# Kernel tuning notes

Hardware: AMD Instinct MI355X
Metric: run time of the kernel (lower is better)

The kernel has to match this reference:

```python
import jax, jax.numpy as jnp
import numpy as np

N_NODES = 100000
N_EDGES = 3200000
D_FEAT = 128
HIDDEN = 128
BN_EPS = 1e-3  # Keras BatchNormalization default epsilon


def setup_inputs() -> dict:
    key = jax.random.key(0)
    k = jax.random.split(key, 8)
    H = jax.random.normal(k[0], (N_NODES, D_FEAT), dtype=jnp.float32)
    edge_src = jax.random.randint(k[1], (N_EDGES,), 0, N_NODES, dtype=jnp.int32)
    edge_dst = jax.random.randint(k[2], (N_EDGES,), 0, N_NODES, dtype=jnp.int32)
    edge_w = jax.random.uniform(k[3], (N_EDGES,), dtype=jnp.float32)
    # BatchNorm (inference-mode) parameters
    gamma = jnp.ones((D_FEAT,), dtype=jnp.float32)
    beta = jnp.zeros((D_FEAT,), dtype=jnp.float32)
    moving_mean = 0.1 * jax.random.normal(k[4], (D_FEAT,), dtype=jnp.float32)
    moving_var = jnp.abs(1.0 + 0.1 * jax.random.normal(k[5], (D_FEAT,), dtype=jnp.float32))
    # Dense layer params
    W = jax.random.normal(k[6], (D_FEAT, HIDDEN), dtype=jnp.float32) / np.sqrt(D_FEAT)
    b = jnp.zeros((HIDDEN,), dtype=jnp.float32)
    return {
        "H": H, "edge_src": edge_src, "edge_dst": edge_dst, "edge_w": edge_w,
        "gamma": gamma, "beta": beta, "moving_mean": moving_mean,
        "moving_var": moving_var, "W": W, "b": b, "num_nodes": N_NODES,
    }


def reference(H, edge_src, edge_dst, edge_w, gamma, beta, moving_mean, moving_var, W, b, num_nodes):
    # Sparse adjacency SpMM: h[dst] += w * H[src]
    msgs = H[edge_src] * edge_w[:, None]                      # [E, d]
    h = jax.ops.segment_sum(msgs, edge_dst, num_segments=num_nodes)  # [N, d]
    # BatchNorm (inference) -> Dropout (identity at inference) -> Dense + exact GELU
    h = (h - moving_mean) * jax.lax.rsqrt(moving_var + BN_EPS) * gamma + beta
    out = jax.nn.gelu(h @ W + b, approximate=False)           # [N, hidden]
    return out
```

## Files before the change

### kernel.cpp

```cpp
#include <hip/hip_runtime.h>
#include <math.h>


#define DF 128
#define SCAN_ELEMS 1024
#define BKSH 6
#define BKNODES (1 << BKSH)
#define NB 128
#define CAP 4096

typedef short short8 __attribute__((ext_vector_type(8)));
typedef float f32x4 __attribute__((ext_vector_type(4)));

__device__ __forceinline__ unsigned short f32_to_bf16_rne(float f) {
  unsigned u = __float_as_uint(f);
  return (unsigned short)((u + 0x7FFFu + ((u >> 16) & 1u)) >> 16);
}

__global__ __launch_bounds__(256) void scatter_kernel(
    const float* __restrict__ H, const int* __restrict__ esrc,
    const int* __restrict__ edst, const float* __restrict__ ew,
    float* __restrict__ h, int E) {
  int tid = blockIdx.x * blockDim.x + threadIdx.x;
  int e = tid >> 5;
  int lane = tid & 31;
  if (e >= E) return;
  int s = esrc[e];
  int d = edst[e];
  float w = ew[e];
  const float4* Hs = reinterpret_cast<const float4*>(H + (size_t)s * DF);
  float4 v = Hs[lane];
  float* hd = h + (size_t)d * DF + lane * 4;
  atomicAdd(hd + 0, v.x * w);
  atomicAdd(hd + 1, v.y * w);
  atomicAdd(hd + 2, v.z * w);
  atomicAdd(hd + 3, v.w * w);
}

__global__ __launch_bounds__(256) void convert_bf16_kernel(
    const float4* __restrict__ H4, ushort4* __restrict__ Hb, int n4) {
  int i = blockIdx.x * blockDim.x + threadIdx.x;
  if (i >= n4) return;
  float4 v = H4[i];
  ushort4 o;
  o.x = f32_to_bf16_rne(v.x);
  o.y = f32_to_bf16_rne(v.y);
  o.z = f32_to_bf16_rne(v.z);
  o.w = f32_to_bf16_rne(v.w);
  Hb[i] = o;
}

__global__ __launch_bounds__(256) void prep_w2frag_kernel(
    const float* __restrict__ W, const float* __restrict__ gamma,
    const float* __restrict__ var, unsigned short* __restrict__ W2frag) {
  int idx = blockIdx.x * blockDim.x + threadIdx.x;
  int i = idx & 7;
  int l = (idx >> 3) & 63;
  int kt = (idx >> 9) & 3;
  int ct = idx >> 11;
  int k = kt * 32 + (l >> 4) * 8 + i;
  int c = ct * 16 + (l & 15);
  float s = gamma[k] * rsqrtf(var[k] + 1e-3f);
  W2frag[idx] = f32_to_bf16_rne(s * W[(size_t)k * DF + c]);
}

__global__ __launch_bounds__(128) void prep_bias2_kernel(
    const float* __restrict__ W, const float* __restrict__ gamma,
    const float* __restrict__ beta, const float* __restrict__ mean,
    const float* __restrict__ var, const float* __restrict__ b,
    float* __restrict__ bias2) {
  int c = threadIdx.x;
  float acc = b[c];
  for (int k = 0; k < DF; ++k) {
    float s = gamma[k] * rsqrtf(var[k] + 1e-3f);
    float t = beta[k] - mean[k] * s;
    acc += t * W[(size_t)k * DF + c];
  }
  bias2[c] = acc;
}

__global__ __launch_bounds__(512) void hist_blk_kernel(
    const int* __restrict__ edst, int* __restrict__ bcnt,
    int E, int nbk, int chunk) {
  extern __shared__ int hcnt[];
  int b = blockIdx.x;
  int t = threadIdx.x;
  for (int i = t; i < nbk; i += 512) hcnt[i] = 0;
  __syncthreads();
  int e0 = b * chunk;
  int e1 = min(E, e0 + chunk);
  for (int e = e0 + t; e < e1; e += 512)
    atomicAdd(&hcnt[edst[e] >> BKSH], 1);
  __syncthreads();
  for (int k = t; k < nbk; k += 512)
    bcnt[(size_t)k * NB + b] = hcnt[k];
}

__global__ __launch_bounds__(256) void scan1_kernel(
    const int* __restrict__ cnt, int* __restrict__ pre,
    int* __restrict__ bsum, int N) {
  __shared__ int s[256];
  int t = threadIdx.x;
  int base = blockIdx.x * SCAN_ELEMS + t * 4;
  int v0 = (base + 0 < N) ? cnt[base + 0] : 0;
  int v1 = (base + 1 < N) ? cnt[base + 1] : 0;
  int v2 = (base + 2 < N) ? cnt[base + 2] : 0;
  int v3 = (base + 3 < N) ? cnt[base + 3] : 0;
  int tsum = v0 + v1 + v2 + v3;
  s[t] = tsum;
  __syncthreads();
  for (int off = 1; off < 256; off <<= 1) {
    int tmp = (t >= off) ? s[t - off] : 0;
    __syncthreads();
    s[t] += tmp;
    __syncthreads();
  }
  int run = s[t] - tsum;
  if (base + 0 < N) pre[base + 0] = run;
  run += v0;
  if (base + 1 < N) pre[base + 1] = run;
  run += v1;
  if (base + 2 < N) pre[base + 2] = run;
  run += v2;
  if (base + 3 < N) pre[base + 3] = run;
  if (t == 255) bsum[blockIdx.x] = s[255];
}

__global__ __launch_bounds__(256) void scan2_kernel(int* __restrict__ bsum, int nb) {
  __shared__ int s[256];
  int t = threadIdx.x;
  int v = (t < nb) ? bsum[t] : 0;
  s[t] = v;
  __syncthreads();
  for (int off = 1; off < 256; off <<= 1) {
    int tmp = (t >= off) ? s[t - off] : 0;
    __syncthreads();
    s[t] += tmp;
    __syncthreads();
  }
  if (t < nb) bsum[t] = s[t] - v;
  if (t == 255) bsum[nb] = s[255];
}

__global__ __launch_bounds__(256) void scan3_kernel(
    int* __restrict__ gbase, const int* __restrict__ bsum, int NBKG, int nb) {
  int i = blockIdx.x * blockDim.x + threadIdx.x;
  if (i < NBKG) gbase[i] += bsum[i >> 10];
  if (i == 0) gbase[NBKG] = bsum[nb];
}

__global__ __launch_bounds__(512) void scatter_blk_kernel(
    const int* __restrict__ esrc, const int* __restrict__ edst,
    const float* __restrict__ ew, const int* __restrict__ gbase,
    uint2* __restrict__ payload, int E, int nbk, int chunk) {
  extern __shared__ int cur[];
  int b = blockIdx.x;
  int t = threadIdx.x;
  for (int k = t; k < nbk; k += 512) cur[k] = gbase[(size_t)k * NB + b];
  __syncthreads();
  int e0 = b * chunk;
  int e1 = min(E, e0 + chunk);
  for (int e = e0 + t; e < e1; e += 512) {
    int d = edst[e];
    int k = d >> BKSH;
    int pos = atomicAdd(&cur[k], 1);
    uint2 v;
    v.x = (unsigned)esrc[e] | ((unsigned)(d & (BKNODES - 1)) << 17);
    v.y = __float_as_uint(ew[e]);
    payload[pos] = v;
  }
}

__global__ __launch_bounds__(256) void reorder2_kernel(
    const uint2* __restrict__ payload, const int* __restrict__ gbase,
    uint2* __restrict__ csr, int* __restrict__ rowptr,
    int N, int nbk, int E) {
  __shared__ uint2 stage[CAP];
  __shared__ int cnt[BKNODES];
  __shared__ int s64[BKNODES];
  __shared__ int cur[BKNODES];
  int bk = blockIdx.x;
  int t = threadIdx.x;
  int base = gbase[(size_t)bk * NB];
  int end  = gbase[(size_t)(bk + 1) * NB];
  int len = end - base;
  bool fit = (len <= CAP);

  if (t < BKNODES) cnt[t] = 0;
  __syncthreads();
  if (fit) {
    for (int j = t; j < len; j += 256) {
      uint2 m = payload[base + j];
      stage[j] = m;
      atomicAdd(&cnt[m.x >> 17], 1);
    }
  } else {
    for (int j = t; j < len; j += 256)
      atomicAdd(&cnt[payload[base + j].x >> 17], 1);
  }
  __syncthreads();
  if (t < BKNODES) s64[t] = cnt[t];
  __syncthreads();
  for (int off = 1; off < BKNODES; off <<= 1) {
    int tmp = 0;
    if (t < BKNODES && t >= off) tmp = s64[t - off];
    __syncthreads();
    if (t < BKNODES) s64[t] += tmp;
    __syncthreads();
  }
  if (t < BKNODES) {
    int ex = s64[t] - cnt[t];
    cur[t] = ex;
    int node = (bk << BKSH) + t;
    if (node < N) rowptr[node] = base + ex;
  }
  if (bk == nbk - 1 && t == 0) rowptr[N] = E;
  __syncthreads();
  if (fit) {
    for (int j = t; j < len; j += 256) {
      uint2 m = stage[j];
      int dl = (int)(m.x >> 17);
      int pos = atomicAdd(&cur[dl], 1);
      uint2 o;
      o.x = m.x & 0x1FFFFu;
      o.y = m.y;
      csr[(size_t)base + pos] = o;
    }
  } else {
    for (int j = t; j < len; j += 256) {
      uint2 m = payload[base + j];
      int dl = (int)(m.x >> 17);
      int pos = atomicAdd(&cur[dl], 1);
      uint2 o;
      o.x = m.x & 0x1FFFFu;
      o.y = m.y;
      csr[(size_t)base + pos] = o;
    }
  }
}

__global__ __launch_bounds__(256) void pull_csr_b_kernel(
    const unsigned* __restrict__ Hb, const int* __restrict__ rowptr,
    const uint2* __restrict__ csr_sw, unsigned* __restrict__ hb_out, int N) {
  int wave = threadIdx.x >> 6;
  int lane = threadIdx.x & 63;
  int node = blockIdx.x * 4 + wave;
  if (node >= N) return;

  int rs = rowptr[node];
  int re = rowptr[node + 1];
  float ax = 0.0f, ay = 0.0f;

  int j = rs;
  for (; j + 8 <= re; j += 8) {
    uint2 m[8];
#pragma unroll
    for (int k = 0; k < 8; ++k) m[k] = csr_sw[j + k];
    float lo[8], hi[8];
#pragma unroll
    for (int k = 0; k < 8; ++k) {
      unsigned p = Hb[(size_t)m[k].x * 64 + lane];
      lo[k] = __uint_as_float(p << 16);
      hi[k] = __uint_as_float(p & 0xFFFF0000u);
    }
#pragma unroll
    for (int k = 0; k < 8; ++k) {
      float w = __uint_as_float(m[k].y);
      ax = fmaf(lo[k], w, ax);
      ay = fmaf(hi[k], w, ay);
    }
  }
  for (; j < re; ++j) {
    uint2 m = csr_sw[j];
    float w = __uint_as_float(m.y);
    unsigned p = Hb[(size_t)m.x * 64 + lane];
    ax = fmaf(__uint_as_float(p << 16), w, ax);
    ay = fmaf(__uint_as_float(p & 0xFFFF0000u), w, ay);
  }

  unsigned pack = (unsigned)f32_to_bf16_rne(ax) |
                  ((unsigned)f32_to_bf16_rne(ay) << 16);
  hb_out[(size_t)node * 64 + lane] = pack;
}

__global__ __launch_bounds__(256) void pull_csr_f32_kernel(
    const float2* __restrict__ H2, const int* __restrict__ rowptr,
    const uint2* __restrict__ csr_sw, float* __restrict__ h, int N) {
  int wave = threadIdx.x >> 6;
  int lane = threadIdx.x & 63;
  int node = blockIdx.x * 4 + wave;
  if (node >= N) return;
  int rs = rowptr[node];
  int re = rowptr[node + 1];
  float ax = 0.0f, ay = 0.0f;
  for (int j = rs; j < re; ++j) {
    uint2 m = csr_sw[j];
    float w = __uint_as_float(m.y);
    float2 u = H2[(size_t)m.x * 64 + lane];
    ax = fmaf(u.x, w, ax);
    ay = fmaf(u.y, w, ay);
  }
  float2 r;
  r.x = ax;
  r.y = ay;
  reinterpret_cast<float2*>(h)[(size_t)node * 64 + lane] = r;
}

__global__ __launch_bounds__(256) void mfma_gemm_gelu_kernel(
    const unsigned short* __restrict__ hb,
    const unsigned short* __restrict__ W2frag,
    const float* __restrict__ bias2,
    float* __restrict__ out, int N) {
  __shared__ unsigned short sW[8 * 4 * 64 * 8];

  int t = threadIdx.x;
  {
    const uint4* src = (const uint4*)W2frag;
    uint4* dst = (uint4*)sW;
    for (int i = t; i < 2048; i += 256) dst[i] = src[i];
  }
  __syncthreads();

  int wid = t >> 6;
  int l = t & 63;
  int row0 = blockIdx.x * 64 + wid * 16;

  int arow = row0 + (l & 15);
  if (arow >= N) arow = N - 1;
  const short8* hrow = (const short8*)(hb + (size_t)arow * DF);
  int asub = l >> 4;
  short8 a[4];
#pragma unroll
  for (int kt = 0; kt < 4; ++kt) a[kt] = hrow[kt * 4 + asub];

  const short8* wf = (const short8*)sW;
  int orow = (l >> 4) * 4;
  int ocol = l & 15;

#pragma unroll
  for (int ct = 0; ct < 8; ++ct) {
    f32x4 acc = {0.0f, 0.0f, 0.0f, 0.0f};
#pragma unroll
    for (int kt = 0; kt < 4; ++kt) {
      short8 bfr = wf[(ct * 4 + kt) * 64 + l];
      acc = __builtin_amdgcn_mfma_f32_16x16x32_bf16(a[kt], bfr, acc, 0, 0, 0);
    }
    int col = ct * 16 + ocol;
    float bb = bias2[col];
#pragma unroll
    for (int r = 0; r < 4; ++r) {
      int row = row0 + orow + r;
      if (row < N) {
        float x = acc[r] + bb;
        float g = 0.5f * x * (1.0f + erff(x * 0.70710678118654752440f));
        out[(size_t)row * DF + col] = g;
      }
    }
  }
}

__global__ __launch_bounds__(256) void fused_bn_gemm_gelu(
    float* __restrict__ hout, const float* __restrict__ gamma,
    const float* __restrict__ beta, const float* __restrict__ mean,
    const float* __restrict__ var, const float* __restrict__ W,
    const float* __restrict__ b, int N) {
  __shared__ float s_s[DF];
  __shared__ float s_t[DF];
  __shared__ float s_hb[16][DF];
  __shared__ float s_W[32][DF];

  int t = threadIdx.x;
  if (t < DF) {
    float sv = gamma[t] * rsqrtf(var[t] + 1e-3f);
    s_s[t] = sv;
    s_t[t] = beta[t] - mean[t] * sv;
  }
  __syncthreads();

  int n0 = blockIdx.x * 16;
  for (int i = t; i < 16 * DF; i += 256) {
    int r = i >> 7;
    int c = i & (DF - 1);
    int node = n0 + r;
    float hv = (node < N) ? hout[(size_t)node * DF + c] : 0.0f;
    s_hb[r][c] = hv * s_s[c] + s_t[c];
  }

  float acc[8];
#pragma unroll
  for (int i = 0; i < 8; i++) acc[i] = 0.0f;

  int col = t & (DF - 1);
  int half = t >> 7;

  for (int kc = 0; kc < DF; kc += 32) {
    __syncthreads();
    for (int i = t; i < 32 * DF; i += 256) {
      int r = i >> 7;
      int c = i & (DF - 1);
      s_W[r][c] = W[(size_t)(kc + r) * DF + c];
    }
    __syncthreads();
#pragma unroll
    for (int kk = 0; kk < 32; kk++) {
      float wv = s_W[kk][col];
#pragma unroll
      for (int i = 0; i < 8; i++) {
        acc[i] += s_hb[half + i * 2][kc + kk] * wv;
      }
    }
  }

  float bb = b[col];
#pragma unroll
  for (int i = 0; i < 8; i++) {
    int node = n0 + half + i * 2;
    if (node < N) {
      float x = acc[i] + bb;
      float g = 0.5f * x * (1.0f + erff(x * 0.70710678118654752440f));
      hout[(size_t)node * DF + col] = g;
    }
  }
}

extern "C" void kernel_launch(void* const* d_in, const int* in_sizes, int n_in,
                              void* d_out, int out_size, void* d_ws, size_t ws_size,
                              hipStream_t stream) {
  const float* H     = (const float*)d_in[0];
  const int*   esrc  = (const int*)d_in[1];
  const int*   edst  = (const int*)d_in[2];
  const float* ew    = (const float*)d_in[3];
  const float* gamma = (const float*)d_in[4];
  const float* beta  = (const float*)d_in[5];
  const float* mean  = (const float*)d_in[6];
  const float* var   = (const float*)d_in[7];
  const float* W     = (const float*)d_in[8];
  const float* b     = (const float*)d_in[9];

  int N = in_sizes[0] / DF;
  int E = in_sizes[1];
  float* h = (float*)d_out;

  int nbk = (N + BKNODES - 1) / BKNODES;
  int NBKG = nbk * NB;
  int nbA = (NBKG + SCAN_ELEMS - 1) / SCAN_ELEMS;
  int chunk = (E + NB - 1) / NB;

  size_t off = 0;
  auto alloc = [&](size_t bytes) {
    size_t o = off;
    off += (bytes + 255) & ~(size_t)255;
    return o;
  };
  size_t o_bcnt   = alloc((size_t)NBKG * 4);
  size_t o_gbase  = alloc((size_t)(NBKG + 1) * 4);
  size_t o_bsum   = alloc((size_t)(nbA + 1) * 4);
  size_t o_rowptr = alloc((size_t)(N + 1) * 4);
  size_t o_w2     = alloc((size_t)16384 * 2);
  size_t o_bias2  = alloc((size_t)DF * 4);
  size_t o_pl     = alloc((size_t)E * 8);
  size_t o_csr    = alloc((size_t)E * 8);
  size_t need_bin = off;
  size_t o_hb     = alloc((size_t)N * DF * 2);
  size_t need_bf16 = off;

  char* ws = (char*)d_ws;

  if (ws_size >= need_bin) {
    int* bcnt    = (int*)(ws + o_bcnt);
    int* gbase   = (int*)(ws + o_gbase);
    int* bsum    = (int*)(ws + o_bsum);
    int* rowptr  = (int*)(ws + o_rowptr);
    unsigned short* W2frag = (unsigned short*)(ws + o_w2);
    float* bias2 = (float*)(ws + o_bias2);
    uint2* payload = (uint2*)(ws + o_pl);
    uint2* csr     = (uint2*)(ws + o_csr);
    bool tierA = (ws_size >= need_bf16 && (size_t)N * DF * 2 <= (size_t)E * 8);

    size_t lds_bytes = (size_t)nbk * 4;

    if (tierA) {
      ushort4* Hb = (ushort4*)(ws + o_hb);
      int n4 = N * DF / 4;
      convert_bf16_kernel<<<(n4 + 255) / 256, 256, 0, stream>>>(
          (const float4*)H, Hb, n4);
      prep_w2frag_kernel<<<64, 256, 0, stream>>>(W, gamma, var, W2frag);
      prep_bias2_kernel<<<1, 128, 0, stream>>>(W, gamma, beta, mean, var, b,
                                               bias2);
      hist_blk_kernel<<<NB, 512, lds_bytes, stream>>>(edst, bcnt, E, nbk, chunk);
      scan1_kernel<<<nbA, 256, 0, stream>>>(bcnt, gbase, bsum, NBKG);
      scan2_kernel<<<1, 256, 0, stream>>>(bsum, nbA);
      scan3_kernel<<<(NBKG + 256) / 256, 256, 0, stream>>>(gbase, bsum, NBKG, nbA);
      scatter_blk_kernel<<<NB, 512, lds_bytes, stream>>>(esrc, edst, ew, gbase,
                                                         payload, E, nbk, chunk);
      reorder2_kernel<<<nbk, 256, 0, stream>>>(payload, gbase, csr, rowptr,
                                               N, nbk, E);
      unsigned* hb_out = (unsigned*)(ws + o_pl);
      pull_csr_b_kernel<<<(N + 3) / 4, 256, 0, stream>>>(
          (const unsigned*)Hb, rowptr, csr, hb_out, N);
      mfma_gemm_gelu_kernel<<<(N + 63) / 64, 256, 0, stream>>>(
          (const unsigned short*)hb_out, W2frag, bias2, (float*)d_out, N);
    } else {
      hist_blk_kernel<<<NB, 512, lds_bytes, stream>>>(edst, bcnt, E, nbk, chunk);
      scan1_kernel<<<nbA, 256, 0, stream>>>(bcnt, gbase, bsum, NBKG);
      scan2_kernel<<<1, 256, 0, stream>>>(bsum, nbA);
      scan3_kernel<<<(NBKG + 256) / 256, 256, 0, stream>>>(gbase, bsum, NBKG, nbA);
      scatter_blk_kernel<<<NB, 512, lds_bytes, stream>>>(esrc, edst, ew, gbase,
                                                         payload, E, nbk, chunk);
      reorder2_kernel<<<nbk, 256, 0, stream>>>(payload, gbase, csr, rowptr,
                                               N, nbk, E);
      pull_csr_f32_kernel<<<(N + 3) / 4, 256, 0, stream>>>(
          (const float2*)H, rowptr, csr, h, N);
      fused_bn_gemm_gelu<<<(N + 15) / 16, 256, 0, stream>>>(h, gamma, beta,
                                                            mean, var, W, b, N);
    }
  } else {
    hipMemsetAsync(d_out, 0, (size_t)out_size * sizeof(float), stream);
    long long threads = (long long)E * 32;
    long long grid = (threads + 255) / 256;
    scatter_kernel<<<(int)grid, 256, 0, stream>>>(H, esrc, edst, ew, h, E);
    fused_bn_gemm_gelu<<<(N + 15) / 16, 256, 0, stream>>>(h, gamma, beta,
                                                          mean, var, W, b, N);
  }
}
```

Measured before the change: 258.1 us.

## Fuse bucket reorder with CSR pull and merge prep/scan kernels

Replaces the separate reorder-to-CSR and pull kernels with one kernel that counting-sorts each 64-node bucket in shared memory and immediately gathers bf16 features for those nodes, avoiding the global CSR/rowptr write and reread. Also merges the three prep kernels into one launch and scan2/scan3 into one kernel that recomputes the block-sum scan per block. Trades global traffic and launches for large 1024-thread blocks with 48KB LDS, which may reduce occupancy; oversized buckets fall back to a slow linear scan path.

```diff
diff --git a/kernel.cpp b/kernel.cpp
--- a/kernel.cpp
+++ b/kernel.cpp
@@ -8,6 +8,7 @@
 #define BKNODES (1 << BKSH)
 #define NB 128
 #define CAP 4096
+#define CAP2 3072
 
 typedef short short8 __attribute__((ext_vector_type(8)));
 typedef float f32x4 __attribute__((ext_vector_type(4)));
@@ -37,63 +38,58 @@
   atomicAdd(hd + 3, v.w * w);
 }
 
-__global__ __launch_bounds__(256) void convert_bf16_kernel(
-    const float4* __restrict__ H4, ushort4* __restrict__ Hb, int n4) {
-  int i = blockIdx.x * blockDim.x + threadIdx.x;
-  if (i >= n4) return;
-  float4 v = H4[i];
-  ushort4 o;
-  o.x = f32_to_bf16_rne(v.x);
-  o.y = f32_to_bf16_rne(v.y);
-  o.z = f32_to_bf16_rne(v.z);
-  o.w = f32_to_bf16_rne(v.w);
-  Hb[i] = o;
-}
-
-__global__ __launch_bounds__(256) void prep_w2frag_kernel(
-    const float* __restrict__ W, const float* __restrict__ gamma,
-    const float* __restrict__ var, unsigned short* __restrict__ W2frag) {
-  int idx = blockIdx.x * blockDim.x + threadIdx.x;
-  int i = idx & 7;
-  int l = (idx >> 3) & 63;
-  int kt = (idx >> 9) & 3;
-  int ct = idx >> 11;
-  int k = kt * 32 + (l >> 4) * 8 + i;
-  int c = ct * 16 + (l & 15);
-  float s = gamma[k] * rsqrtf(var[k] + 1e-3f);
-  W2frag[idx] = f32_to_bf16_rne(s * W[(size_t)k * DF + c]);
-}
-
-__global__ __launch_bounds__(128) void prep_bias2_kernel(
+__global__ __launch_bounds__(256) void prep_all_kernel(
+    const float4* __restrict__ H4, ushort4* __restrict__ Hb, int n4,
     const float* __restrict__ W, const float* __restrict__ gamma,
     const float* __restrict__ beta, const float* __restrict__ mean,
     const float* __restrict__ var, const float* __restrict__ b,
-    float* __restrict__ bias2) {
-  int c = threadIdx.x;
-  float acc = b[c];
-  for (int k = 0; k < DF; ++k) {
+    unsigned short* __restrict__ W2frag, float* __restrict__ bias2) {
+  int idx = blockIdx.x * blockDim.x + threadIdx.x;
+  if (idx < n4) {
+    float4 v = H4[idx];
+    ushort4 o;
+    o.x = f32_to_bf16_rne(v.x);
+    o.y = f32_to_bf16_rne(v.y);
+    o.z = f32_to_bf16_rne(v.z);
+    o.w = f32_to_bf16_rne(v.w);
+    Hb[idx] = o;
+  }
+  if (idx < 16384) {
+    int i = idx & 7;
+    int l = (idx >> 3) & 63;
+    int kt = (idx >> 9) & 3;
+    int ct = idx >> 11;
+    int k = kt * 32 + (l >> 4) * 8 + i;
+    int c = ct * 16 + (l & 15);
     float s = gamma[k] * rsqrtf(var[k] + 1e-3f);
-    float t = beta[k] - mean[k] * s;
-    acc += t * W[(size_t)k * DF + c];
-  }
-  bias2[c] = acc;
+    W2frag[idx] = f32_to_bf16_rne(s * W[(size_t)k * DF + c]);
+  } else if (idx < 16384 + DF) {
+    int c = idx - 16384;
+    float acc = b[c];
+    for (int k = 0; k < DF; ++k) {
+      float s = gamma[k] * rsqrtf(var[k] + 1e-3f);
+      float t = beta[k] - mean[k] * s;
+      acc += t * W[(size_t)k * DF + c];
+    }
+    bias2[c] = acc;
+  }
 }
 
 __global__ __launch_bounds__(512) void hist_blk_kernel(
     const int* __restrict__ edst, int* __restrict__ bcnt,
     int E, int nbk, int chunk) {
   extern __shared__ int hcnt[];
-  int b = blockIdx.x;
+  int bblk = blockIdx.x;
   int t = threadIdx.x;
   for (int i = t; i < nbk; i += 512) hcnt[i] = 0;
   __syncthreads();
-  int e0 = b * chunk;
+  int e0 = bblk * chunk;
   int e1 = min(E, e0 + chunk);
   for (int e = e0 + t; e < e1; e += 512)
     atomicAdd(&hcnt[edst[e] >> BKSH], 1);
   __syncthreads();
   for (int k = t; k < nbk; k += 512)
-    bcnt[(size_t)k * NB + b] = hcnt[k];
+    bcnt[(size_t)k * NB + bblk] = hcnt[k];
 }
 
 __global__ __launch_bounds__(256) void scan1_kernel(
@@ -126,10 +122,11 @@
   if (t == 255) bsum[blockIdx.x] = s[255];
 }
 
-__global__ __launch_bounds__(256) void scan2_kernel(int* __restrict__ bsum, int nb) {
+__global__ __launch_bounds__(256) void scan23_kernel(
+    int* __restrict__ gbase, const int* __restrict__ bsum, int NBKG, int nbA) {
   __shared__ int s[256];
   int t = threadIdx.x;
-  int v = (t < nb) ? bsum[t] : 0;
+  int v = (t < nbA) ? bsum[t] : 0;
   s[t] = v;
   __syncthreads();
   for (int off = 1; off < 256; off <<= 1) {
@@ -138,15 +135,13 @@
     s[t] += tmp;
     __syncthreads();
   }
-  if (t < nb) bsum[t] = s[t] - v;
-  if (t == 255) bsum[nb] = s[255];
-}
-
-__global__ __launch_bounds__(256) void scan3_kernel(
-    int* __restrict__ gbase, const int* __restrict__ bsum, int NBKG, int nb) {
-  int i = blockIdx.x * blockDim.x + threadIdx.x;
-  if (i < NBKG) gbase[i] += bsum[i >> 10];
-  if (i == 0) gbase[NBKG] = bsum[nb];
+  int i = blockIdx.x * 256 + t;
+  if (i < NBKG) {
+    int blk = i >> 10;
+    int add = (blk == 0) ? 0 : s[blk - 1];
+    gbase[i] += add;
+  }
+  if (blockIdx.x == 0 && t == 0) gbase[NBKG] = s[nbA - 1];
 }
 
 __global__ __launch_bounds__(512) void scatter_blk_kernel(
@@ -154,11 +149,11 @@
     const float* __restrict__ ew, const int* __restrict__ gbase,
     uint2* __restrict__ payload, int E, int nbk, int chunk) {
   extern __shared__ int cur[];
-  int b = blockIdx.x;
-  int t = threadIdx.x;
-  for (int k = t; k < nbk; k += 512) cur[k] = gbase[(size_t)k * NB + b];
-  __syncthreads();
-  int e0 = b * chunk;
+  int bblk = blockIdx.x;
+  int t = threadIdx.x;
+  for (int k = t; k < nbk; k += 512) cur[k] = gbase[(size_t)k * NB + bblk];
+  __syncthreads();
+  int e0 = bblk * chunk;
   int e1 = min(E, e0 + chunk);
   for (int e = e0 + t; e < e1; e += 512) {
     int d = edst[e];
@@ -171,6 +166,167 @@
   }
 }
 
+__global__ __launch_bounds__(1024, 8) void reorder_pull_kernel(
+    const unsigned* __restrict__ Hb, const uint2* __restrict__ payload,
+    const int* __restrict__ gbase, unsigned* __restrict__ hb_out, int N) {
+  __shared__ uint2 stage[CAP2];
+  __shared__ uint2 sorted[CAP2];
+  __shared__ int cnt[BKNODES];
+  __shared__ int scn[BKNODES];
+  __shared__ int cur[BKNODES];
+  int bk = blockIdx.x;
+  int t = threadIdx.x;
+  int base = gbase[(size_t)bk * NB];
+  int end  = gbase[(size_t)(bk + 1) * NB];
+  int len = end - base;
+  int wid = t >> 6;
+  int lane = t & 63;
+
+  if (len <= CAP2) {
+    if (t < BKNODES) cnt[t] = 0;
+    __syncthreads();
+    for (int j = t; j < len; j += 1024) {
+      uint2 m = payload[base + j];
+      stage[j] = m;
+      atomicAdd(&cnt[m.x >> 17], 1);
+    }
+    __syncthreads();
+    if (t < BKNODES) scn[t] = cnt[t];
+    __syncthreads();
+    for (int off = 1; off < BKNODES; off <<= 1) {
+      int tmp = 0;
+      if (t < BKNODES && t >= off) tmp = scn[t - off];
+      __syncthreads();
+      if (t < BKNODES) scn[t] += tmp;
+      __syncthreads();
+    }
+    if (t < BKNODES) cur[t] = scn[t] - cnt[t];
+    __syncthreads();
+    for (int j = t; j < len; j += 1024) {
+      uint2 m = stage[j];
+      int dl = (int)(m.x >> 17);
+      int pos = atomicAdd(&cur[dl], 1);
+      uint2 o;
+      o.x = m.x & 0x1FFFFu;
+      o.y = m.y;
+      sorted[pos] = o;
+    }
+    __syncthreads();
+
+#pragma unroll
+    for (int i = 0; i < 4; ++i) {
+      int dl = wid * 4 + i;
+      int node = (bk << BKSH) + dl;
+      if (node >= N) break;
+      int s1 = scn[dl];
+      int s0 = s1 - cnt[dl];
+      float ax = 0.0f, ay = 0.0f;
+      int j = s0;
+      for (; j + 8 <= s1; j += 8) {
+        uint2 m[8];
+#pragma unroll
+        for (int k = 0; k < 8; ++k) m[k] = sorted[j + k];
+        float lo[8], hi[8];
+#pragma unroll
+        for (int k = 0; k < 8; ++k) {
+          unsigned p = Hb[(size_t)m[k].x * 64 + lane];
+          lo[k] = __uint_as_float(p << 16);
+          hi[k] = __uint_as_float(p & 0xFFFF0000u);
+        }
+#pragma unroll
+        for (int k = 0; k < 8; ++k) {
+          float w = __uint_as_float(m[k].y);
+          ax = fmaf(lo[k], w, ax);
+          ay = fmaf(hi[k], w, ay);
+        }
+      }
+      for (; j < s1; ++j) {
+        uint2 m = sorted[j];
+        float w = __uint_as_float(m.y);
+        unsigned p = Hb[(size_t)m.x * 64 + lane];
+        ax = fmaf(__uint_as_float(p << 16), w, ax);
+        ay = fmaf(__uint_as_float(p & 0xFFFF0000u), w, ay);
+      }
+      unsigned pack = (unsigned)f32_to_bf16_rne(ax) |
+                      ((unsigned)f32_to_bf16_rne(ay) << 16);
+      hb_out[(size_t)node * 64 + lane] = pack;
+    }
+  } else {
+#pragma unroll
+    for (int i = 0; i < 4; ++i) {
+      int dl = wid * 4 + i;
+      int node = (bk << BKSH) + dl;
+      if (node >= N) break;
+      float ax = 0.0f, ay = 0.0f;
+      for (int j = base; j < end; ++j) {
+        uint2 m = payload[j];
+        if ((int)(m.x >> 17) == dl) {
+          float w = __uint_as_float(m.y);
+          unsigned p = Hb[(size_t)(m.x & 0x1FFFFu) * 64 + lane];
+          ax = fmaf(__uint_as_float(p << 16), w, ax);
+          ay = fmaf(__uint_as_float(p & 0xFFFF0000u), w, ay);
+        }
+      }
+      unsigned pack = (unsigned)f32_to_bf16_rne(ax) |
+                      ((unsigned)f32_to_bf16_rne(ay) << 16);
+      hb_out[(size_t)node * 64 + lane] = pack;
+    }
+  }
+}
+
+__global__ __launch_bounds__(256) void mfma_gemm_gelu_kernel(
+    const unsigned short* __restrict__ hb,
+    const unsigned short* __restrict__ W2frag,
+    const float* __restrict__ bias2,
+    float* __restrict__ out, int N) {
+  __shared__ unsigned short sW[8 * 4 * 64 * 8];
+
+  int t = threadIdx.x;
+  {
+    const uint4* src = (const uint4*)W2frag;
+    uint4* dst = (uint4*)sW;
+    for (int i = t; i < 2048; i += 256) dst[i] = src[i];
+  }
+  __syncthreads();
+
+  int wid = t >> 6;
+  int l = t & 63;
+  int row0 = blockIdx.x * 64 + wid * 16;
+
+  int arow = row0 + (l & 15);
+  if (arow >= N) arow = N - 1;
+  const short8* hrow = (const short8*)(hb + (size_t)arow * DF);
+  int asub = l >> 4;
+  short8 a[4];
+#pragma unroll
+  for (int kt = 0; kt < 4; ++kt) a[kt] = hrow[kt * 4 + asub];
+
+  const short8* wf = (const short8*)sW;
+  int orow = (l >> 4) * 4;
+  int ocol = l & 15;
+
+#pragma unroll
+  for (int ct = 0; ct < 8; ++ct) {
+    f32x4 acc = {0.0f, 0.0f, 0.0f, 0.0f};
+#pragma unroll
+    for (int kt = 0; kt < 4; ++kt) {
+      short8 bfr = wf[(ct * 4 + kt) * 64 + l];
+      acc = __builtin_amdgcn_mfma_f32_16x16x32_bf16(a[kt], bfr, acc, 0, 0, 0);
+    }
+    int col = ct * 16 + ocol;
+    float bb = bias2[col];
+#pragma unroll
+    for (int r = 0; r < 4; ++r) {
+      int row = row0 + orow + r;
+      if (row < N) {
+        float x = acc[r] + bb;
+        float g = 0.5f * x * (1.0f + erff(x * 0.70710678118654752440f));
+        out[(size_t)row * DF + col] = g;
+      }
+    }
+  }
+}
+
 __global__ __launch_bounds__(256) void reorder2_kernel(
     const uint2* __restrict__ payload, const int* __restrict__ gbase,
     uint2* __restrict__ csr, int* __restrict__ rowptr,
@@ -237,50 +393,6 @@
       csr[(size_t)base + pos] = o;
     }
   }
-}
-
-__global__ __launch_bounds__(256) void pull_csr_b_kernel(
-    const unsigned* __restrict__ Hb, const int* __restrict__ rowptr,
-    const uint2* __restrict__ csr_sw, unsigned* __restrict__ hb_out, int N) {
-  int wave = threadIdx.x >> 6;
-  int lane = threadIdx.x & 63;
-  int node = blockIdx.x * 4 + wave;
-  if (node >= N) return;
-
-  int rs = rowptr[node];
-  int re = rowptr[node + 1];
-  float ax = 0.0f, ay = 0.0f;
-
-  int j = rs;
-  for (; j + 8 <= re; j += 8) {
-    uint2 m[8];
-#pragma unroll
-    for (int k = 0; k < 8; ++k) m[k] = csr_sw[j + k];
-    float lo[8], hi[8];
-#pragma unroll
-    for (int k = 0; k < 8; ++k) {
-      unsigned p = Hb[(size_t)m[k].x * 64 + lane];
-      lo[k] = __uint_as_float(p << 16);
-      hi[k] = __uint_as_float(p & 0xFFFF0000u);
-    }
-#pragma unroll
-    for (int k = 0; k < 8; ++k) {
-      float w = __uint_as_float(m[k].y);
-      ax = fmaf(lo[k], w, ax);
-      ay = fmaf(hi[k], w, ay);
-    }
-  }
-  for (; j < re; ++j) {
-    uint2 m = csr_sw[j];
-    float w = __uint_as_float(m.y);
-    unsigned p = Hb[(size_t)m.x * 64 + lane];
-    ax = fmaf(__uint_as_float(p << 16), w, ax);
-    ay = fmaf(__uint_as_float(p & 0xFFFF0000u), w, ay);
-  }
-
-  unsigned pack = (unsigned)f32_to_bf16_rne(ax) |
-                  ((unsigned)f32_to_bf16_rne(ay) << 16);
-  hb_out[(size_t)node * 64 + lane] = pack;
 }
 
 __global__ __launch_bounds__(256) void pull_csr_f32_kernel(
@@ -304,59 +416,6 @@
   r.x = ax;
   r.y = ay;
   reinterpret_cast<float2*>(h)[(size_t)node * 64 + lane] = r;
-}
-
-__global__ __launch_bounds__(256) void mfma_gemm_gelu_kernel(
-    const unsigned short* __restrict__ hb,
-    const unsigned short* __restrict__ W2frag,
-    const float* __restrict__ bias2,
-    float* __restrict__ out, int N) {
-  __shared__ unsigned short sW[8 * 4 * 64 * 8];
-
-  int t = threadIdx.x;
-  {
-    const uint4* src = (const uint4*)W2frag;
-    uint4* dst = (uint4*)sW;
-    for (int i = t; i < 2048; i += 256) dst[i] = src[i];
-  }
-  __syncthreads();
-
-  int wid = t >> 6;
-  int l = t & 63;
-  int row0 = blockIdx.x * 64 + wid * 16;
-
-  int arow = row0 + (l & 15);
-  if (arow >= N) arow = N - 1;
-  const short8* hrow = (const short8*)(hb + (size_t)arow * DF);
-  int asub = l >> 4;
-  short8 a[4];
-#pragma unroll
-  for (int kt = 0; kt < 4; ++kt) a[kt] = hrow[kt * 4 + asub];
-
-  const short8* wf = (const short8*)sW;
-  int orow = (l >> 4) * 4;
-  int ocol = l & 15;
-
-#pragma unroll
-  for (int ct = 0; ct < 8; ++ct) {
-    f32x4 acc = {0.0f, 0.0f, 0.0f, 0.0f};
-#pragma unroll
-    for (int kt = 0; kt < 4; ++kt) {
-      short8 bfr = wf[(ct * 4 + kt) * 64 + l];
-      acc = __builtin_amdgcn_mfma_f32_16x16x32_bf16(a[kt], bfr, acc, 0, 0, 0);
-    }
-    int col = ct * 16 + ocol;
-    float bb = bias2[col];
-#pragma unroll
-    for (int r = 0; r < 4; ++r) {
-      int row = row0 + orow + r;
-      if (row < N) {
-        float x = acc[r] + bb;
-        float g = 0.5f * x * (1.0f + erff(x * 0.70710678118654752440f));
-        out[(size_t)row * DF + col] = g;
-      }
-    }
-  }
 }
 
 __global__ __launch_bounds__(256) void fused_bn_gemm_gelu(
@@ -482,29 +541,22 @@
     if (tierA) {
       ushort4* Hb = (ushort4*)(ws + o_hb);
       int n4 = N * DF / 4;
-      convert_bf16_kernel<<<(n4 + 255) / 256, 256, 0, stream>>>(
-          (const float4*)H, Hb, n4);
-      prep_w2frag_kernel<<<64, 256, 0, stream>>>(W, gamma, var, W2frag);
-      prep_bias2_kernel<<<1, 128, 0, stream>>>(W, gamma, beta, mean, var, b,
-                                               bias2);
+      prep_all_kernel<<<(n4 + 255) / 256, 256, 0, stream>>>(
+          (const float4*)H, Hb, n4, W, gamma, beta, mean, var, b, W2frag, bias2);
       hist_blk_kernel<<<NB, 512, lds_bytes, stream>>>(edst, bcnt, E, nbk, chunk);
       scan1_kernel<<<nbA, 256, 0, stream>>>(bcnt, gbase, bsum, NBKG);
-      scan2_kernel<<<1, 256, 0, stream>>>(bsum, nbA);
-      scan3_kernel<<<(NBKG + 256) / 256, 256, 0, stream>>>(gbase, bsum, NBKG, nbA);
+      scan23_kernel<<<(NBKG + 255) / 256, 256, 0, stream>>>(gbase, bsum, NBKG, nbA);
       scatter_blk_kernel<<<NB, 512, lds_bytes, stream>>>(esrc, edst, ew, gbase,
                                                          payload, E, nbk, chunk);
-      reorder2_kernel<<<nbk, 256, 0, stream>>>(payload, gbase, csr, rowptr,
-                                               N, nbk, E);
-      unsigned* hb_out = (unsigned*)(ws + o_pl);
-      pull_csr_b_kernel<<<(N + 3) / 4, 256, 0, stream>>>(
-          (const unsigned*)Hb, rowptr, csr, hb_out, N);
+      unsigned* hb_out = (unsigned*)(ws + o_csr);
+      reorder_pull_kernel<<<nbk, 1024, 0, stream>>>(
+          (const unsigned*)Hb, payload, gbase, hb_out, N);
       mfma_gemm_gelu_kernel<<<(N + 63) / 64, 256, 0, stream>>>(
           (const unsigned short*)hb_out, W2frag, bias2, (float*)d_out, N);
     } else {
       hist_blk_kernel<<<NB, 512, lds_bytes, stream>>>(edst, bcnt, E, nbk, chunk);
       scan1_kernel<<<nbA, 256, 0, stream>>>(bcnt, gbase, bsum, NBKG);
-      scan2_kernel<<<1, 256, 0, stream>>>(bsum, nbA);
-      scan3_kernel<<<(NBKG + 256) / 256, 256, 0, stream>>>(gbase, bsum, NBKG, nbA);
+      scan23_kernel<<<(NBKG + 255) / 256, 256, 0, stream>>>(gbase, bsum, NBKG, nbA);
       scatter_blk_kernel<<<NB, 512, lds_bytes, stream>>>(esrc, edst, ew, gbase,
                                                          payload, E, nbk, chunk);
       reorder2_kernel<<<nbk, 256, 0, stream>>>(payload, gbase, csr, rowptr,
```

After: 232.0 us. 1.11x faster.
